# Kernel optimization log

Hardware: AMD Instinct MI355X
Metric: run time of the kernel (lower is better)

The kernel has to match this reference:

```python
import jax, jax.numpy as jnp
import numpy as np

H = 2048  # LSTM units


def lstm_last(x, Wk, Wr, b):
    # x: [B,T,F]; Wk: [F,4H]; Wr: [H,4H]; b: [4H]
    # Precompute input projections for all timesteps (one big GEMM).
    xz = jnp.einsum('btf,fg->btg', x, Wk) + b  # [B,T,4H]

    def step(carry, zt):
        h, c = carry
        z = zt + h @ Wr  # [B,4H]
        i, f, g, o = jnp.split(z, 4, axis=-1)  # keras gate order i,f,c,o
        i = jax.nn.sigmoid(i)
        f = jax.nn.sigmoid(f)
        g = jnp.tanh(g)
        o = jax.nn.sigmoid(o)
        c = f * c + i * g
        h = o * jnp.tanh(c)
        return (h, c), None

    B = x.shape[0]
    h0 = jnp.zeros((B, H), x.dtype)
    (h, _), _ = jax.lax.scan(step, (h0, h0), jnp.swapaxes(xz, 0, 1))
    return h  # last hidden state [B,H] (return_sequences=False)


def setup_inputs() -> dict:
    key = jax.random.key(0)
    ks = jax.random.split(key, 8)
    B, T, F = 64, 1024, 256
    x = jax.random.normal(ks[0], (B, T, F), dtype=jnp.float32)
    Wk = jax.random.normal(ks[1], (F, 4 * H), dtype=jnp.float32) * 0.05
    Wr = jax.random.normal(ks[2], (H, 4 * H), dtype=jnp.float32) * 0.02
    b = jnp.zeros((4 * H,), dtype=jnp.float32).at[H:2 * H].set(1.0)  # unit_forget_bias
    Wd = jax.random.normal(ks[3], (H, 512), dtype=jnp.float32) * 0.05
    bd = jnp.zeros((512,), dtype=jnp.float32)
    Wo = jax.random.normal(ks[4], (512, 1), dtype=jnp.float32) * 0.05
    bo = jnp.zeros((1,), dtype=jnp.float32)
    return {"x": x, "Wk": Wk, "Wr": Wr, "b": b, "Wd": Wd, "bd": bd, "Wo": Wo, "bo": bo}


def reference(x, Wk, Wr, b, Wd, bd, Wo, bo):
    # Dropout evaluated in inference mode (identity) for a deterministic baseline.
    h = lstm_last(x, Wk, Wr, b)          # [B,2048]
    y = jax.nn.relu(h @ Wd + bd)          # [B,512]
    y = jax.nn.relu(y @ Wo + bo)          # [B,1]
    return y
```

## Files before the change

### kernel.cpp

```cpp
#include <hip/hip_runtime.h>

#define TT   1024
#define BB   64
#define FF   256
#define HH   2048
#define G4   8192
#define KTOT 2304
#define KP   2312
#define NBLK 256
#define NTHR 512
#define NWAVE 8
#define RR   4
#define RMASK (RR - 1)
#define WL_BYTES (32 * KP * 2)
#define SMEM_BYTES WL_BYTES
#define HSLOT16 (NBLK * 512)
#define HBYTES ((size_t)HSLOT16 * 2)
#define POLL_CAP (1 << 17)

typedef __attribute__((ext_vector_type(8))) short bf16x8;
typedef __attribute__((ext_vector_type(4))) float f32x4;

__device__ __forceinline__ unsigned short f2bf(float f) {
  unsigned u = __float_as_uint(f);
  u += 0x7FFFu + ((u >> 16) & 1u);
  return (unsigned short)(u >> 16);
}
__device__ __forceinline__ float bf2f(unsigned short b) {
  return __uint_as_float((unsigned)b << 16);
}
__device__ __forceinline__ float sigm(float x) { return 1.0f / (1.0f + __expf(-x)); }
__device__ __forceinline__ float tanhfast(float x) {
  x = fminf(fmaxf(x, -15.0f), 15.0f);
  float e = __expf(2.0f * x);
  return (e - 1.0f) / (e + 1.0f);
}

__global__ void __launch_bounds__(NTHR, 2) lstm_persist(
    const float* __restrict__ x,
    const float* __restrict__ Wk,
    const float* __restrict__ Wr,
    const float* __restrict__ bias,
    unsigned short* __restrict__ hbufs,
    unsigned* __restrict__ stamps)
{
  extern __shared__ char smem[];
  unsigned short* Wl = (unsigned short*)smem;
  float* zl = (float*)smem;

  const int tid = threadIdx.x;
  const int j = blockIdx.x;
  const int lane = tid & 63;
  const int wid  = tid >> 6;
  const int cl   = lane & 15;
  const int ko   = (lane >> 4) * 8;
  const int rg   = lane >> 4;

  for (int idx = tid; idx < 32 * KTOT; idx += NTHR) {
    int cc = idx & 31;
    int k  = idx >> 5;
    int zc = (cc >> 3) * HH + j * 8 + (cc & 7);
    float wv = (k < FF) ? Wk[(size_t)k * G4 + zc] : Wr[(size_t)(k - FF) * G4 + zc];
    Wl[cc * KP + k] = f2bf(wv);
  }
  __syncthreads();

  bf16x8 bfr[2][9];
  #pragma unroll
  for (int n = 0; n < 2; ++n) {
    #pragma unroll
    for (int s = 0; s < 9; ++s) {
      int kbase = (s == 0) ? (wid * 32)
                           : (FF + wid * 256 + (s - 1) * 32);
      bfr[n][s] = *(const bf16x8*)(Wl + (n * 16 + cl) * KP + kbase + ko);
    }
  }
  __syncthreads();

  const int hc2  = (tid & 3) * 2;
  const int bb   = tid >> 2;
  const int col0 = j * 8 + hc2;
  const float bi0 = bias[col0],          bi1 = bias[col0 + 1];
  const float bf0 = bias[HH + col0],     bf1 = bias[HH + col0 + 1];
  const float bg0 = bias[2*HH + col0],   bg1 = bias[2*HH + col0 + 1];
  const float bo0 = bias[3*HH + col0],   bo1 = bias[3*HH + col0 + 1];
  float cA = 0.0f, cB = 0.0f;

  f32x4 acc[4][2];

#define XPART(TS) do {                                                        \
    _Pragma("unroll")                                                         \
    for (int m = 0; m < 4; ++m) {                                             \
      acc[m][0] = (f32x4){0.f,0.f,0.f,0.f};                                   \
      acc[m][1] = (f32x4){0.f,0.f,0.f,0.f};                                   \
    }                                                                         \
    {                                                                         \
      const int kx = wid * 32 + ko;                                           \
      _Pragma("unroll")                                                       \
      for (int m = 0; m < 4; ++m) {                                           \
        const float* xr = x + ((size_t)(m*16 + cl) * TT + (TS)) * FF + kx;    \
        const float4 v0 = *(const float4*)(xr);                               \
        const float4 v1 = *(const float4*)(xr + 4);                           \
        bf16x8 a;                                                             \
        a[0] = (short)f2bf(v0.x); a[1] = (short)f2bf(v0.y);                   \
        a[2] = (short)f2bf(v0.z); a[3] = (short)f2bf(v0.w);                   \
        a[4] = (short)f2bf(v1.x); a[5] = (short)f2bf(v1.y);                   \
        a[6] = (short)f2bf(v1.z); a[7] = (short)f2bf(v1.w);                   \
        acc[m][0] = __builtin_amdgcn_mfma_f32_16x16x32_bf16(a, bfr[0][0], acc[m][0], 0, 0, 0); \
        acc[m][1] = __builtin_amdgcn_mfma_f32_16x16x32_bf16(a, bfr[1][0], acc[m][1], 0, 0, 0); \
      }                                                                       \
    }                                                                         \
  } while (0)

  XPART(0);

  for (int t = 0; t < TT; ++t) {
    if ((t & RMASK) == 0) {
      if (tid < 64) __builtin_amdgcn_fence(__ATOMIC_ACQUIRE, "agent");
      __syncthreads();
    }

    if (t > 0) {
      const unsigned* sp = stamps + wid * 32 + (lane & 31);
      for (int it = 0; it < POLL_CAP; ++it) {
        unsigned v = __hip_atomic_load(sp, __ATOMIC_RELAXED, __HIP_MEMORY_SCOPE_AGENT);
        if (__all((int)(v >= (unsigned)t))) break;
      }
      asm volatile("" ::: "memory");
      __builtin_amdgcn_sched_barrier(0);
    }

    const unsigned short* hb = hbufs + (size_t)(t & RMASK) * HSLOT16;
    #pragma unroll
    for (int s = 1; s < 9; ++s) {
      const int kh = wid * 256 + (s - 1) * 32 + ko;
      const unsigned short* hkb = hb + ((size_t)(kh >> 3) << 9);
      #pragma unroll
      for (int m = 0; m < 4; ++m) {
        bf16x8 a = *(const bf16x8*)(hkb + (size_t)(m * 16 + cl) * 8);
        acc[m][0] = __builtin_amdgcn_mfma_f32_16x16x32_bf16(a, bfr[0][s], acc[m][0], 0, 0, 0);
        acc[m][1] = __builtin_amdgcn_mfma_f32_16x16x32_bf16(a, bfr[1][s], acc[m][1], 0, 0, 0);
      }
    }

    #pragma unroll
    for (int m = 0; m < 4; ++m)
      #pragma unroll
      for (int n = 0; n < 2; ++n)
        *(f32x4*)(zl + (size_t)(wid * 32 + n * 16 + cl) * 68 + m * 16 + rg * 4) = acc[m][n];
    __syncthreads();

    if (tid < 256) {
      float zs[8];
      #pragma unroll
      for (int g = 0; g < 4; ++g) {
        float s0 = 0.f, s1 = 0.f;
        #pragma unroll
        for (int w = 0; w < NWAVE; ++w) {
          s0 += zl[(size_t)(w * 32 + g * 8 + hc2)     * 68 + bb];
          s1 += zl[(size_t)(w * 32 + g * 8 + hc2 + 1) * 68 + bb];
        }
        zs[2*g] = s0; zs[2*g+1] = s1;
      }
      float iA = sigm(zs[0] + bi0), iB = sigm(zs[1] + bi1);
      float fA = sigm(zs[2] + bf0), fB = sigm(zs[3] + bf1);
      float gA = tanhfast(zs[4] + bg0), gB = tanhfast(zs[5] + bg1);
      float oA = sigm(zs[6] + bo0), oB = sigm(zs[7] + bo1);
      cA = fA * cA + iA * gA;
      cB = fB * cB + iB * gB;
      float hA = oA * tanhfast(cA);
      float hB = oB * tanhfast(cB);
      unsigned* hw = (unsigned*)(hbufs + (size_t)((t + 1) & RMASK) * HSLOT16)
                     + j * 256 + tid;
      unsigned hp = (unsigned)f2bf(hA) | ((unsigned)f2bf(hB) << 16);
      __hip_atomic_store(hw, hp, __ATOMIC_RELAXED, __HIP_MEMORY_SCOPE_AGENT);
    }

    if (t + 1 < TT) {
      asm volatile("s_waitcnt vmcnt(0)" ::: "memory");
      __syncthreads();
      if (tid == 0)
        __hip_atomic_store(&stamps[j], (unsigned)(t + 1),
                           __ATOMIC_RELAXED, __HIP_MEMORY_SCOPE_AGENT);
      asm volatile("" ::: "memory");
      XPART(t + 1);
    }
  }
#undef XPART
}

__global__ void dense_fused(const unsigned short* __restrict__ hT,
                            const float* __restrict__ Wd,
                            const float* __restrict__ bd,
                            const float* __restrict__ Wo,
                            const float* __restrict__ bo,
                            float* __restrict__ out) {
  __shared__ float hrow[HH];
  __shared__ float y1s[512];
  __shared__ float red[256];
  const int b = blockIdx.x, tid = threadIdx.x;
  for (int k = tid; k < HH; k += 256)
    hrow[k] = bf2f(hT[((size_t)(k >> 3) << 9) + b * 8 + (k & 7)]);
  __syncthreads();
  for (int c = tid; c < 512; c += 256) {
    float acc = bd[c];
    #pragma unroll 8
    for (int k = 0; k < HH; ++k) acc = fmaf(hrow[k], Wd[(size_t)k * 512 + c], acc);
    y1s[c] = fmaxf(acc, 0.0f);
  }
  __syncthreads();
  red[tid] = y1s[tid] * Wo[tid] + y1s[tid + 256] * Wo[tid + 256];
  __syncthreads();
  for (int st = 128; st > 0; st >>= 1) {
    if (tid < st) red[tid] += red[tid + st];
    __syncthreads();
  }
  if (tid == 0) out[b] = fmaxf(red[0] + bo[0], 0.0f);
}

extern "C" void kernel_launch(void* const* d_in, const int* in_sizes, int n_in,
                              void* d_out, int out_size, void* d_ws, size_t ws_size,
                              hipStream_t stream) {
  const float* x    = (const float*)d_in[0];
  const float* Wk   = (const float*)d_in[1];
  const float* Wr   = (const float*)d_in[2];
  const float* bias = (const float*)d_in[3];
  const float* Wd   = (const float*)d_in[4];
  const float* bd   = (const float*)d_in[5];
  const float* Wo   = (const float*)d_in[6];
  const float* bo   = (const float*)d_in[7];
  float* out = (float*)d_out;

  char* w = (char*)d_ws;
  unsigned short* hbufs = (unsigned short*)w;
  unsigned* stamps      = (unsigned*)(w + RR * HBYTES);

  hipMemsetAsync(hbufs, 0, HBYTES, stream);
  hipMemsetAsync(stamps, 0, NBLK * 4, stream);

  hipFuncSetAttribute((const void*)lstm_persist,
                      hipFuncAttributeMaxDynamicSharedMemorySize, SMEM_BYTES);

  void* args[] = { (void*)&x, (void*)&Wk, (void*)&Wr, (void*)&bias,
                   (void*)&hbufs, (void*)&stamps };
  hipLaunchCooperativeKernel((const void*)lstm_persist, dim3(NBLK), dim3(NTHR),
                             args, SMEM_BYTES, stream);

  dense_fused<<<dim3(BB), dim3(256), 0, stream>>>(hbufs ,
                                                  Wd, bd, Wo, bo, out);
}
```

Before: 9.409 ms.

## Split each block into two batch-half teams with LDS counter barriers and per-team stamps

Each block's 8 waves are split into two independent teams, each owning 32 batch rows, with 4 waves per team splitting the K dimension. __syncthreads is replaced by LDS atomic-counter spin barriers scoped to each team, and there are separate global stamps per team, so each batch half proceeds without waiting for the other half across the grid. The partial-sum buffer is double-buffered by timestep parity, and the next-step input projection is overlapped on idle waves. In exchange, each wave keeps twice as many weight fragments in registers, the spin barriers rely on relaxed LDS atomics, and the h-buffer layout changes.

```diff
diff --git a/kernel.cpp b/kernel.cpp
--- a/kernel.cpp
+++ b/kernel.cpp
@@ -9,14 +9,15 @@
 #define KP   2312
 #define NBLK 256
 #define NTHR 512
-#define NWAVE 8
 #define RR   4
 #define RMASK (RR - 1)
 #define WL_BYTES (32 * KP * 2)
+#define ZL_FLOATS (2 * 2 * 4 * 32 * 36)
 #define SMEM_BYTES WL_BYTES
 #define HSLOT16 (NBLK * 512)
 #define HBYTES ((size_t)HSLOT16 * 2)
-#define POLL_CAP (1 << 17)
+#define POLL_CAP (1 << 16)
+#define SPIN_CAP (1 << 17)
 
 typedef __attribute__((ext_vector_type(8))) short bf16x8;
 typedef __attribute__((ext_vector_type(4))) float f32x4;
@@ -34,6 +35,20 @@
   x = fminf(fmaxf(x, -15.0f), 15.0f);
   float e = __expf(2.0f * x);
   return (e - 1.0f) / (e + 1.0f);
+}
+
+__device__ __forceinline__ void team_arrive(unsigned* c, int lane) {
+  asm volatile("s_waitcnt lgkmcnt(0)" ::: "memory");
+  if (lane == 0)
+    __hip_atomic_fetch_add(c, 1u, __ATOMIC_RELAXED, __HIP_MEMORY_SCOPE_WORKGROUP);
+}
+__device__ __forceinline__ void team_spin(unsigned* c, unsigned tgt) {
+  for (int it = 0; it < SPIN_CAP; ++it) {
+    if (__hip_atomic_load(c, __ATOMIC_RELAXED, __HIP_MEMORY_SCOPE_WORKGROUP) >= tgt)
+      break;
+  }
+  asm volatile("" ::: "memory");
+  __builtin_amdgcn_sched_barrier(0);
 }
 
 __global__ void __launch_bounds__(NTHR, 2) lstm_persist(
@@ -47,14 +62,17 @@
   extern __shared__ char smem[];
   unsigned short* Wl = (unsigned short*)smem;
   float* zl = (float*)smem;
+  unsigned* ctr = (unsigned*)(smem + ZL_FLOATS * 4);
 
   const int tid = threadIdx.x;
   const int j = blockIdx.x;
   const int lane = tid & 63;
   const int wid  = tid >> 6;
+  const int tm   = wid >> 2;
+  const int kq   = wid & 3;
   const int cl   = lane & 15;
   const int ko   = (lane >> 4) * 8;
-  const int rg   = lane >> 4;
+  const int rg4  = lane >> 4;
 
   for (int idx = tid; idx < 32 * KTOT; idx += NTHR) {
     int cc = idx & 31;
@@ -65,40 +83,52 @@
   }
   __syncthreads();
 
-  bf16x8 bfr[2][9];
+  bf16x8 bfr[2][18];
   #pragma unroll
   for (int n = 0; n < 2; ++n) {
     #pragma unroll
-    for (int s = 0; s < 9; ++s) {
-      int kbase = (s == 0) ? (wid * 32)
-                           : (FF + wid * 256 + (s - 1) * 32);
+    for (int s = 0; s < 18; ++s) {
+      int kbase = (s < 2) ? (kq * 64 + s * 32)
+                          : (FF + kq * 512 + (s - 2) * 32);
       bfr[n][s] = *(const bf16x8*)(Wl + (n * 16 + cl) * KP + kbase + ko);
     }
   }
   __syncthreads();
-
-  const int hc2  = (tid & 3) * 2;
-  const int bb   = tid >> 2;
-  const int col0 = j * 8 + hc2;
-  const float bi0 = bias[col0],          bi1 = bias[col0 + 1];
-  const float bf0 = bias[HH + col0],     bf1 = bias[HH + col0 + 1];
-  const float bg0 = bias[2*HH + col0],   bg1 = bias[2*HH + col0 + 1];
-  const float bo0 = bias[3*HH + col0],   bo1 = bias[3*HH + col0 + 1];
+  if (tid < 4) ctr[tid] = 0;
+  __syncthreads();
+
+  const int g    = (kq & 1) * 64 + lane;
+  const int grow = g >> 2;
+  const int gpr  = g & 3;
+  const int c0   = j * 8 + gpr * 2;
+  const float bi0 = bias[c0],          bi1 = bias[c0 + 1];
+  const float bf0 = bias[HH + c0],     bf1 = bias[HH + c0 + 1];
+  const float bg0 = bias[2*HH + c0],   bg1 = bias[2*HH + c0 + 1];
+  const float bo0 = bias[3*HH + c0],   bo1 = bias[3*HH + c0 + 1];
   float cA = 0.0f, cB = 0.0f;
 
-  f32x4 acc[4][2];
+  unsigned* ctrA = ctr + tm * 2;
+  unsigned* ctrB = ctr + tm * 2 + 1;
+  unsigned* mystamps = stamps + tm * NBLK;
+
+  f32x4 acc[2][2];
+
+#define ZLI(PAR, Q, COL, ROW) \
+  (((((PAR) * 2 + tm) * 4 + (Q)) * 32 + (COL)) * 36 + (ROW))
 
 #define XPART(TS) do {                                                        \
     _Pragma("unroll")                                                         \
-    for (int m = 0; m < 4; ++m) {                                             \
+    for (int m = 0; m < 2; ++m) {                                             \
       acc[m][0] = (f32x4){0.f,0.f,0.f,0.f};                                   \
       acc[m][1] = (f32x4){0.f,0.f,0.f,0.f};                                   \
     }                                                                         \
-    {                                                                         \
-      const int kx = wid * 32 + ko;                                           \
+    _Pragma("unroll")                                                         \
+    for (int s = 0; s < 2; ++s) {                                             \
+      const int kx = kq * 64 + s * 32 + ko;                                   \
       _Pragma("unroll")                                                       \
-      for (int m = 0; m < 4; ++m) {                                           \
-        const float* xr = x + ((size_t)(m*16 + cl) * TT + (TS)) * FF + kx;    \
+      for (int m = 0; m < 2; ++m) {                                           \
+        const int row = tm * 32 + m * 16 + cl;                                \
+        const float* xr = x + ((size_t)row * TT + (TS)) * FF + kx;            \
         const float4 v0 = *(const float4*)(xr);                               \
         const float4 v1 = *(const float4*)(xr + 4);                           \
         bf16x8 a;                                                             \
@@ -106,8 +136,8 @@
         a[2] = (short)f2bf(v0.z); a[3] = (short)f2bf(v0.w);                   \
         a[4] = (short)f2bf(v1.x); a[5] = (short)f2bf(v1.y);                   \
         a[6] = (short)f2bf(v1.z); a[7] = (short)f2bf(v1.w);                   \
-        acc[m][0] = __builtin_amdgcn_mfma_f32_16x16x32_bf16(a, bfr[0][0], acc[m][0], 0, 0, 0); \
-        acc[m][1] = __builtin_amdgcn_mfma_f32_16x16x32_bf16(a, bfr[1][0], acc[m][1], 0, 0, 0); \
+        acc[m][0] = __builtin_amdgcn_mfma_f32_16x16x32_bf16(a, bfr[0][s], acc[m][0], 0, 0, 0); \
+        acc[m][1] = __builtin_amdgcn_mfma_f32_16x16x32_bf16(a, bfr[1][s], acc[m][1], 0, 0, 0); \
       }                                                                       \
     }                                                                         \
   } while (0)
@@ -115,13 +145,8 @@
   XPART(0);
 
   for (int t = 0; t < TT; ++t) {
-    if ((t & RMASK) == 0) {
-      if (tid < 64) __builtin_amdgcn_fence(__ATOMIC_ACQUIRE, "agent");
-      __syncthreads();
-    }
-
     if (t > 0) {
-      const unsigned* sp = stamps + wid * 32 + (lane & 31);
+      const unsigned* sp = mystamps + kq * 64 + lane;
       for (int it = 0; it < POLL_CAP; ++it) {
         unsigned v = __hip_atomic_load(sp, __ATOMIC_RELAXED, __HIP_MEMORY_SCOPE_AGENT);
         if (__all((int)(v >= (unsigned)t))) break;
@@ -129,38 +154,43 @@
       asm volatile("" ::: "memory");
       __builtin_amdgcn_sched_barrier(0);
     }
+    if ((t & RMASK) == 0)
+      __builtin_amdgcn_fence(__ATOMIC_ACQUIRE, "agent");
 
     const unsigned short* hb = hbufs + (size_t)(t & RMASK) * HSLOT16;
     #pragma unroll
-    for (int s = 1; s < 9; ++s) {
-      const int kh = wid * 256 + (s - 1) * 32 + ko;
-      const unsigned short* hkb = hb + ((size_t)(kh >> 3) << 9);
+    for (int s = 0; s < 16; ++s) {
+      const int kh = kq * 512 + s * 32 + ko;
+      const unsigned short* cb = hb + ((size_t)(kh >> 3) << 9) + tm * 256;
       #pragma unroll
-      for (int m = 0; m < 4; ++m) {
-        bf16x8 a = *(const bf16x8*)(hkb + (size_t)(m * 16 + cl) * 8);
-        acc[m][0] = __builtin_amdgcn_mfma_f32_16x16x32_bf16(a, bfr[0][s], acc[m][0], 0, 0, 0);
-        acc[m][1] = __builtin_amdgcn_mfma_f32_16x16x32_bf16(a, bfr[1][s], acc[m][1], 0, 0, 0);
+      for (int m = 0; m < 2; ++m) {
+        bf16x8 a = *(const bf16x8*)(cb + (m * 16 + cl) * 8);
+        acc[m][0] = __builtin_amdgcn_mfma_f32_16x16x32_bf16(a, bfr[0][2 + s], acc[m][0], 0, 0, 0);
+        acc[m][1] = __builtin_amdgcn_mfma_f32_16x16x32_bf16(a, bfr[1][2 + s], acc[m][1], 0, 0, 0);
       }
     }
 
+    const int par = t & 1;
     #pragma unroll
-    for (int m = 0; m < 4; ++m)
+    for (int m = 0; m < 2; ++m)
       #pragma unroll
       for (int n = 0; n < 2; ++n)
-        *(f32x4*)(zl + (size_t)(wid * 32 + n * 16 + cl) * 68 + m * 16 + rg * 4) = acc[m][n];
-    __syncthreads();
-
-    if (tid < 256) {
+        *(f32x4*)(zl + ZLI(par, kq, n * 16 + cl, m * 16 + rg4 * 4)) = acc[m][n];
+
+    team_arrive(ctrA, lane);
+    team_spin(ctrA, 4u * (unsigned)(t + 1));
+
+    if (kq < 2) {
       float zs[8];
       #pragma unroll
-      for (int g = 0; g < 4; ++g) {
+      for (int gg = 0; gg < 4; ++gg) {
         float s0 = 0.f, s1 = 0.f;
         #pragma unroll
-        for (int w = 0; w < NWAVE; ++w) {
-          s0 += zl[(size_t)(w * 32 + g * 8 + hc2)     * 68 + bb];
-          s1 += zl[(size_t)(w * 32 + g * 8 + hc2 + 1) * 68 + bb];
+        for (int q = 0; q < 4; ++q) {
+          s0 += zl[ZLI(par, q, gg * 8 + gpr * 2,     grow)];
+          s1 += zl[ZLI(par, q, gg * 8 + gpr * 2 + 1, grow)];
         }
-        zs[2*g] = s0; zs[2*g+1] = s1;
+        zs[2*gg] = s0; zs[2*gg+1] = s1;
       }
       float iA = sigm(zs[0] + bi0), iB = sigm(zs[1] + bi1);
       float fA = sigm(zs[2] + bf0), fB = sigm(zs[3] + bf1);
@@ -171,22 +201,26 @@
       float hA = oA * tanhfast(cA);
       float hB = oB * tanhfast(cB);
       unsigned* hw = (unsigned*)(hbufs + (size_t)((t + 1) & RMASK) * HSLOT16)
-                     + j * 256 + tid;
+                     + j * 256 + tm * 128 + grow * 4 + gpr;
       unsigned hp = (unsigned)f2bf(hA) | ((unsigned)f2bf(hB) << 16);
       __hip_atomic_store(hw, hp, __ATOMIC_RELAXED, __HIP_MEMORY_SCOPE_AGENT);
+      asm volatile("s_waitcnt vmcnt(0)" ::: "memory");
+    } else if (t + 1 < TT) {
+      XPART(t + 1);
     }
 
     if (t + 1 < TT) {
-      asm volatile("s_waitcnt vmcnt(0)" ::: "memory");
-      __syncthreads();
-      if (tid == 0)
-        __hip_atomic_store(&stamps[j], (unsigned)(t + 1),
+      team_arrive(ctrB, lane);
+      team_spin(ctrB, 4u * (unsigned)(t + 1));
+      if (kq == 0 && lane == 0)
+        __hip_atomic_store(&mystamps[j], (unsigned)(t + 1),
                            __ATOMIC_RELAXED, __HIP_MEMORY_SCOPE_AGENT);
       asm volatile("" ::: "memory");
-      XPART(t + 1);
+      if (kq < 2) XPART(t + 1);
     }
   }
 #undef XPART
+#undef ZLI
 }
 
 __global__ void dense_fused(const unsigned short* __restrict__ hT,
@@ -200,7 +234,7 @@
   __shared__ float red[256];
   const int b = blockIdx.x, tid = threadIdx.x;
   for (int k = tid; k < HH; k += 256)
-    hrow[k] = bf2f(hT[((size_t)(k >> 3) << 9) + b * 8 + (k & 7)]);
+    hrow[k] = bf2f(hT[((size_t)(k >> 3) << 9) + ((b >> 5) << 8) + (b & 31) * 8 + (k & 7)]);
   __syncthreads();
   for (int c = tid; c < 512; c += 256) {
     float acc = bd[c];
@@ -236,7 +270,7 @@
   unsigned* stamps      = (unsigned*)(w + RR * HBYTES);
 
   hipMemsetAsync(hbufs, 0, HBYTES, stream);
-  hipMemsetAsync(stamps, 0, NBLK * 4, stream);
+  hipMemsetAsync(stamps, 0, 2 * NBLK * 4, stream);
 
   hipFuncSetAttribute((const void*)lstm_persist,
                       hipFuncAttributeMaxDynamicSharedMemorySize, SMEM_BYTES);
```

Measured after the change: 17.16 ms. 82.4% more time.

## Replicate per-block step stamps per XCD and deepen the h ring buffer

Applied to the files above, without the earlier changes.

Each block now writes its step stamp into 8 replicated stamp arrays. Pollers read only the copy indexed by their XCC_ID hardware register, which spreads the spin-polling traffic that 256 blocks aim at one set of cache lines across separate address sets. The hidden-state ring grows from 4 to 8 slots when the workspace allows, via a runtime rmask, so the acquire fence and block barrier run half as often. The cost is 8 stamp stores per block per step and a larger workspace footprint.

```diff
diff --git a/kernel.cpp b/kernel.cpp
--- a/kernel.cpp
+++ b/kernel.cpp
@@ -10,12 +10,11 @@
 #define NBLK 256
 #define NTHR 512
 #define NWAVE 8
-#define RR   4
-#define RMASK (RR - 1)
 #define WL_BYTES (32 * KP * 2)
 #define SMEM_BYTES WL_BYTES
 #define HSLOT16 (NBLK * 512)
 #define HBYTES ((size_t)HSLOT16 * 2)
+#define NREP 8
 #define POLL_CAP (1 << 17)
 
 typedef __attribute__((ext_vector_type(8))) short bf16x8;
@@ -42,7 +41,8 @@
     const float* __restrict__ Wr,
     const float* __restrict__ bias,
     unsigned short* __restrict__ hbufs,
-    unsigned* __restrict__ stamps)
+    unsigned* __restrict__ stamps,
+    int rmask)
 {
   extern __shared__ char smem[];
   unsigned short* Wl = (unsigned short*)smem;
@@ -55,6 +55,10 @@
   const int cl   = lane & 15;
   const int ko   = (lane >> 4) * 8;
   const int rg   = lane >> 4;
+
+  unsigned xcd;
+  asm("s_getreg_b32 %0, hwreg(HW_REG_XCC_ID)" : "=s"(xcd));
+  xcd &= (NREP - 1);
 
   for (int idx = tid; idx < 32 * KTOT; idx += NTHR) {
     int cc = idx & 31;
@@ -115,13 +119,13 @@
   XPART(0);
 
   for (int t = 0; t < TT; ++t) {
-    if ((t & RMASK) == 0) {
+    if ((t & rmask) == 0) {
       if (tid < 64) __builtin_amdgcn_fence(__ATOMIC_ACQUIRE, "agent");
       __syncthreads();
     }
 
     if (t > 0) {
-      const unsigned* sp = stamps + wid * 32 + (lane & 31);
+      const unsigned* sp = stamps + (size_t)xcd * NBLK + wid * 32 + (lane & 31);
       for (int it = 0; it < POLL_CAP; ++it) {
         unsigned v = __hip_atomic_load(sp, __ATOMIC_RELAXED, __HIP_MEMORY_SCOPE_AGENT);
         if (__all((int)(v >= (unsigned)t))) break;
@@ -130,7 +134,7 @@
       __builtin_amdgcn_sched_barrier(0);
     }
 
-    const unsigned short* hb = hbufs + (size_t)(t & RMASK) * HSLOT16;
+    const unsigned short* hb = hbufs + (size_t)(t & rmask) * HSLOT16;
     #pragma unroll
     for (int s = 1; s < 9; ++s) {
       const int kh = wid * 256 + (s - 1) * 32 + ko;
@@ -170,7 +174,7 @@
       cB = fB * cB + iB * gB;
       float hA = oA * tanhfast(cA);
       float hB = oB * tanhfast(cB);
-      unsigned* hw = (unsigned*)(hbufs + (size_t)((t + 1) & RMASK) * HSLOT16)
+      unsigned* hw = (unsigned*)(hbufs + (size_t)((t + 1) & rmask) * HSLOT16)
                      + j * 256 + tid;
       unsigned hp = (unsigned)f2bf(hA) | ((unsigned)f2bf(hB) << 16);
       __hip_atomic_store(hw, hp, __ATOMIC_RELAXED, __HIP_MEMORY_SCOPE_AGENT);
@@ -179,8 +183,8 @@
     if (t + 1 < TT) {
       asm volatile("s_waitcnt vmcnt(0)" ::: "memory");
       __syncthreads();
-      if (tid == 0)
-        __hip_atomic_store(&stamps[j], (unsigned)(t + 1),
+      if (tid < NREP)
+        __hip_atomic_store(&stamps[(size_t)tid * NBLK + j], (unsigned)(t + 1),
                            __ATOMIC_RELAXED, __HIP_MEMORY_SCOPE_AGENT);
       asm volatile("" ::: "memory");
       XPART(t + 1);
@@ -231,18 +235,23 @@
   const float* bo   = (const float*)d_in[7];
   float* out = (float*)d_out;
 
+  const size_t stamp_bytes = NREP * NBLK * sizeof(unsigned);
+  int R = 8;
+  if ((size_t)R * HBYTES + stamp_bytes > ws_size) R = 4;
+  const int rmask = R - 1;
+
   char* w = (char*)d_ws;
   unsigned short* hbufs = (unsigned short*)w;
-  unsigned* stamps      = (unsigned*)(w + RR * HBYTES);
+  unsigned* stamps      = (unsigned*)(w + (size_t)R * HBYTES);
 
   hipMemsetAsync(hbufs, 0, HBYTES, stream);
-  hipMemsetAsync(stamps, 0, NBLK * 4, stream);
+  hipMemsetAsync(stamps, 0, stamp_bytes, stream);
 
   hipFuncSetAttribute((const void*)lstm_persist,
                       hipFuncAttributeMaxDynamicSharedMemorySize, SMEM_BYTES);
 
   void* args[] = { (void*)&x, (void*)&Wk, (void*)&Wr, (void*)&bias,
-                   (void*)&hbufs, (void*)&stamps };
+                   (void*)&hbufs, (void*)&stamps, (void*)&rmask };
   hipLaunchCooperativeKernel((const void*)lstm_persist, dim3(NBLK), dim3(NTHR),
                              args, SMEM_BYTES, stream);
 
```

New measurement: 9.358 ms (median of 2 runs). No clear change (-0.5%).
